# Kernel optimization log

Measured on AMD Instinct MI355X. Metric: run time of the kernel, lower is better.

## Reference

```python
import jax, jax.numpy as jnp
import numpy as np
from jax import lax

STRIDE = (1, 1)
PADDING = ((1, 1), (1, 1))


@jax.custom_vjp
def ternary_quantize(w):
    """Quantize OIHW weights to {-1,0,+1} with per-output-channel scale alpha."""
    abs_w = jnp.abs(w)
    delta = 0.7 * abs_w.mean(axis=(1, 2, 3), keepdims=True)          # [O,1,1,1]
    ternary = jnp.where(w > delta, 1.0, jnp.where(w < -delta, -1.0, 0.0)).astype(w.dtype)
    mask = ternary != 0
    count = jnp.maximum(mask.sum(axis=(1, 2, 3), keepdims=True), 1).astype(w.dtype)
    alpha = (abs_w * mask.astype(w.dtype)).sum(axis=(1, 2, 3), keepdims=True) / count
    return ternary, alpha


def _tq_fwd(w):
    return ternary_quantize(w), w


def _tq_bwd(w, grads):
    g_ternary, _g_alpha = grads  # STE: grad_alpha is discarded
    g = jnp.where(jnp.abs(w) > 1.0, 0.0, g_ternary)
    return (g,)


ternary_quantize.defvjp(_tq_fwd, _tq_bwd)


def setup_inputs() -> dict:
    key = jax.random.key(0)
    kx, kw = jax.random.split(key)
    x = jax.random.normal(kx, (32, 256, 56, 56), dtype=jnp.float32)
    # kaiming_normal fan_out: std = sqrt(2 / (out_ch * kH * kW))
    std = np.sqrt(2.0 / (256 * 3 * 3)).astype(np.float32)
    weight = jax.random.normal(kw, (256, 256, 3, 3), dtype=jnp.float32) * std
    return {"x": x, "weight": weight}


def reference(x, weight):
    ternary, alpha = ternary_quantize(weight)
    scaled_w = alpha * ternary  # values in {-alpha_o, 0, +alpha_o}
    return lax.conv_general_dilated(
        x, scaled_w,
        window_strides=STRIDE,
        padding=PADDING,
        dimension_numbers=("NCHW", "OIHW", "NCHW"),
    )
```

## Files before the change

### kernel.cpp

```cpp
#include <hip/hip_runtime.h>
#include <hip/hip_bf16.h>

typedef unsigned short u16;
typedef __bf16 bf16x8 __attribute__((ext_vector_type(8)));
typedef float f32x4 __attribute__((ext_vector_type(4)));
typedef u16 u16x8 __attribute__((ext_vector_type(8)));

__device__ __forceinline__ u16 f2bf(float f) {
    __bf16 h = (__bf16)f;
    return __builtin_bit_cast(unsigned short, h);
}

__device__ __forceinline__ void gl_lds16(const u16* g, u16* l) {
    __builtin_amdgcn_global_load_lds(
        (const __attribute__((address_space(1))) void*)g,
        (__attribute__((address_space(3))) void*)l, 16, 0, 0);
}

__device__ __forceinline__ void hard_barrier() {
    asm volatile("s_waitcnt vmcnt(0) lgkmcnt(0)" ::: "memory");
    __builtin_amdgcn_sched_barrier(0);
    __syncthreads();
}

__global__ __launch_bounds__(256) void prep_kernel(
        const float* __restrict__ x, const float* __restrict__ w,
        u16* __restrict__ xp, u16* __restrict__ wp,
        float* __restrict__ alpha) {
    __shared__ double red[4];
    __shared__ double red2[4];
    __shared__ int    redc[4];

    int bid = blockIdx.x;
    int t = threadIdx.x;

    if (bid < 256) {
        int o = bid;
        const float* wo = w + (size_t)o * 2304;
        float v[9];
        double asum = 0.0;
        #pragma unroll
        for (int i = 0; i < 9; ++i) { v[i] = wo[t * 9 + i]; asum += fabs((double)v[i]); }
        #pragma unroll
        for (int off = 32; off > 0; off >>= 1) asum += __shfl_down(asum, off, 64);
        int wv = t >> 6, lane = t & 63;
        if (lane == 0) red[wv] = asum;
        __syncthreads();
        double delta = 0.7 * ((red[0] + red[1] + red[2] + red[3]) / 2304.0);

        int mt = o >> 7, ol = o & 127;
        int ks = (t >> 3) & 7, c = t & 7;
        double msum = 0.0; int cnt = 0;
        #pragma unroll
        for (int i = 0; i < 9; ++i) {
            double f = (double)v[i];
            float tv = 0.f;
            if (f > delta) tv = 1.f;
            else if (f < -delta) tv = -1.f;
            if (tv != 0.f) { msum += fabs(f); cnt++; }
            int kc = i * 4 + (t >> 6);
            wp[((((size_t)mt * 36 + kc) * 8 + ks) * 128 + ol) * 8 + c] = f2bf(tv);
        }
        #pragma unroll
        for (int off = 32; off > 0; off >>= 1) {
            msum += __shfl_down(msum, off, 64);
            cnt  += __shfl_down(cnt,  off, 64);
        }
        if (lane == 0) { red2[wv] = msum; redc[wv] = cnt; }
        __syncthreads();
        if (t == 0) {
            double ms = red2[0] + red2[1] + red2[2] + red2[3];
            int cn = redc[0] + redc[1] + redc[2] + redc[3];
            alpha[o] = (float)(ms / (double)(cn > 0 ? cn : 1));
        }
        return;
    }

    int pbid = bid - 256;
    int img  = pbid & 31;
    int cihi = (pbid >> 5) & 31;
    int z    = pbid >> 10;

    if (z == 3 && t >= 16) {
        int bt = t - 16;
        if (bt < 228) {
            int hp, wl;
            if (bt < 58)       { hp = 0;            wl = bt; }
            else if (bt < 116) { hp = 57;           wl = bt - 58; }
            else if (bt < 172) { hp = bt - 116 + 1; wl = 0; }
            else               { hp = bt - 172 + 1; wl = 57; }
            u16x8 zv = {};
            *(u16x8*)(xp + (((size_t)(img * 32 + cihi) * 58 + hp) * 58 + wl) * 8) = zv;
        }
        return;
    }

    int slot = z * 256 + t;
    if (slot >= 784) return;
    int p = slot * 4;
    int h = p / 56, wq = p - h * 56;
    const float* xb = x + ((size_t)(img * 256 + cihi * 8)) * 3136 + p;
    f32x4 v[8];
    #pragma unroll
    for (int j = 0; j < 8; ++j) v[j] = *(const f32x4*)(xb + (size_t)j * 3136);
    u16* ob = xp + (((size_t)(img * 32 + cihi) * 58 + (h + 1)) * 58 + (wq + 1)) * 8;
    #pragma unroll
    for (int k = 0; k < 4; ++k) {
        u16x8 ov;
        #pragma unroll
        for (int j = 0; j < 8; ++j) ov[j] = f2bf(v[j][k]);
        *(u16x8*)(ob + k * 8) = ov;
    }
}

__global__ __launch_bounds__(256) void conv_gemm(
        const u16* __restrict__ Wp, const u16* __restrict__ Xp,
        const float* __restrict__ alpha, float* __restrict__ out) {
    __shared__ u16 lsA[8 * 128 * 8];
    __shared__ u16 lsB[8 * 128 * 8];

    int bid = blockIdx.x;
    int xcd = bid & 7, idx = bid >> 3;
    int mt = idx & 1;
    unsigned nt = (unsigned)(xcd * 98 + (idx >> 1));
    int o_base = mt * 128;
    unsigned sp_base = nt * 128u;

    int t = threadIdx.x;
    int lane = t & 63, wave = t >> 6;
    int wm = (wave >> 1) * 64, wn = (wave & 1) * 64;

    const u16* aTile = Wp + (size_t)mt * 294912;

    unsigned sp0 = sp_base + (unsigned)lane;
    unsigned sp1 = sp0 + 64u;
    unsigned img0 = sp0 / 3136u, rem0 = sp0 - img0 * 3136u;
    unsigned oh0 = rem0 / 56u,   ow0 = rem0 - oh0 * 56u;
    unsigned img1 = sp1 / 3136u, rem1 = sp1 - img1 * 3136u;
    unsigned oh1 = rem1 / 56u,   ow1 = rem1 - oh1 * 56u;
    const u16* bB0 = Xp + ((size_t)(img0 * 32) * 58 + oh0) * 58 * 8 + ow0 * 8;
    const u16* bB1 = Xp + ((size_t)(img1 * 32) * 58 + oh1) * 58 * 8 + ow1 * 8;

    int s0 = wave * 2, s1 = s0 + 1;
    u16* dB00 = lsB + (s0 * 128) * 8;
    u16* dB01 = lsB + (s0 * 128 + 64) * 8;
    u16* dB10 = lsB + (s1 * 128) * 8;
    u16* dB11 = lsB + (s1 * 128 + 64) * 8;

    f32x4 acc[4][4] = {};
    int row16 = lane & 15, quad = lane >> 4;

    for (int kc = 0; kc < 36; ++kc) {
        int f  = kc >> 2;
        int kh = f / 3, kw = f - kh * 3;
        int ci8 = (kc & 3) * 8;
        unsigned bhw = (unsigned)kh * 464u + (unsigned)kw * 8u;
        unsigned bo0 = (unsigned)(ci8 + s0) * 26912u + bhw;
        unsigned bo1 = (unsigned)(ci8 + s1) * 26912u + bhw;
        const u16* aC = aTile + kc * 8192;

        #pragma unroll
        for (int q = 0; q < 4; ++q) {
            int seg = wave * 4 + q;
            gl_lds16(aC + seg * 512 + lane * 8, lsA + seg * 512);
        }
        gl_lds16(bB0 + bo0, dB00);
        gl_lds16(bB1 + bo0, dB01);
        gl_lds16(bB0 + bo1, dB10);
        gl_lds16(bB1 + bo1, dB11);

        hard_barrier();

        #pragma unroll
        for (int kk = 0; kk < 2; ++kk) {
            int ks = kk * 4 + quad;
            bf16x8 af[4], bfr[4];
            #pragma unroll
            for (int i = 0; i < 4; ++i)
                af[i] = *(const bf16x8*)&lsA[(ks * 128 + wm + i * 16 + row16) * 8];
            #pragma unroll
            for (int j = 0; j < 4; ++j)
                bfr[j] = *(const bf16x8*)&lsB[(ks * 128 + wn + j * 16 + row16) * 8];
            #pragma unroll
            for (int i = 0; i < 4; ++i)
                #pragma unroll
                for (int j = 0; j < 4; ++j)
                    acc[i][j] = __builtin_amdgcn_mfma_f32_16x16x32_bf16(
                                    af[i], bfr[j], acc[i][j], 0, 0, 0);
        }

        hard_barrier();
    }

    int col = lane & 15;
    float al[4][4];
    #pragma unroll
    for (int i = 0; i < 4; ++i)
        #pragma unroll
        for (int rg = 0; rg < 4; ++rg)
            al[i][rg] = alpha[o_base + wm + i * 16 + quad * 4 + rg];

    #pragma unroll
    for (int j = 0; j < 4; ++j) {
        unsigned sp = sp_base + (unsigned)(wn + j * 16 + col);
        unsigned img = sp / 3136u;
        unsigned spi = sp - img * 3136u;
        float* ob = out + (size_t)img * 256 * 3136 + spi;
        #pragma unroll
        for (int i = 0; i < 4; ++i) {
            int o = o_base + wm + i * 16 + quad * 4;
            #pragma unroll
            for (int rg = 0; rg < 4; ++rg)
                ob[(size_t)(o + rg) * 3136] = acc[i][j][rg] * al[i][rg];
        }
    }
}

extern "C" void kernel_launch(void* const* d_in, const int* in_sizes, int n_in,
                              void* d_out, int out_size, void* d_ws, size_t ws_size,
                              hipStream_t stream) {
    const float* x = (const float*)d_in[0];
    const float* w = (const float*)d_in[1];
    float* out = (float*)d_out;

    char* ws = (char*)d_ws;
    u16*   xp    = (u16*)ws;
    u16*   wp    = (u16*)(ws + 55115776);
    float* alpha = (float*)(ws + 55115776 + 1179648);

    prep_kernel<<<4352, 256, 0, stream>>>(x, w, xp, wp, alpha);
    conv_gemm<<<784 * 2, 256, 0, stream>>>(wp, xp, alpha, out);
}
```

Baseline: 348.3 us.

## Double-buffer LDS tiles to overlap global loads with MFMA compute

Splits the A and B shared-memory tiles into two buffers. The global-to-LDS loads for the next K chunk are issued before the MFMAs on the current chunk, and each iteration ends with one barrier instead of two. The goal is to hide global load latency behind compute. It doubles LDS use to 64KB per block, which may lower occupancy. The barrier still waits on vmcnt(0), so the overlap only lasts for the duration of the compute.

```diff
diff --git a/kernel.cpp b/kernel.cpp
--- a/kernel.cpp
+++ b/kernel.cpp
@@ -116,8 +116,8 @@
 __global__ __launch_bounds__(256) void conv_gemm(
         const u16* __restrict__ Wp, const u16* __restrict__ Xp,
         const float* __restrict__ alpha, float* __restrict__ out) {
-    __shared__ u16 lsA[8 * 128 * 8];
-    __shared__ u16 lsB[8 * 128 * 8];
+    __shared__ u16 lsA[2][8 * 128 * 8];
+    __shared__ u16 lsB[2][8 * 128 * 8];
 
     int bid = blockIdx.x;
     int xcd = bid & 7, idx = bid >> 3;
@@ -142,15 +142,11 @@
     const u16* bB1 = Xp + ((size_t)(img1 * 32) * 58 + oh1) * 58 * 8 + ow1 * 8;
 
     int s0 = wave * 2, s1 = s0 + 1;
-    u16* dB00 = lsB + (s0 * 128) * 8;
-    u16* dB01 = lsB + (s0 * 128 + 64) * 8;
-    u16* dB10 = lsB + (s1 * 128) * 8;
-    u16* dB11 = lsB + (s1 * 128 + 64) * 8;
 
     f32x4 acc[4][4] = {};
     int row16 = lane & 15, quad = lane >> 4;
 
-    for (int kc = 0; kc < 36; ++kc) {
+    auto stage = [&](int kc, int buf) {
         int f  = kc >> 2;
         int kh = f / 3, kw = f - kh * 3;
         int ci8 = (kc & 3) * 8;
@@ -158,29 +154,36 @@
         unsigned bo0 = (unsigned)(ci8 + s0) * 26912u + bhw;
         unsigned bo1 = (unsigned)(ci8 + s1) * 26912u + bhw;
         const u16* aC = aTile + kc * 8192;
-
         #pragma unroll
         for (int q = 0; q < 4; ++q) {
             int seg = wave * 4 + q;
-            gl_lds16(aC + seg * 512 + lane * 8, lsA + seg * 512);
-        }
-        gl_lds16(bB0 + bo0, dB00);
-        gl_lds16(bB1 + bo0, dB01);
-        gl_lds16(bB0 + bo1, dB10);
-        gl_lds16(bB1 + bo1, dB11);
-
-        hard_barrier();
-
+            gl_lds16(aC + seg * 512 + lane * 8, &lsA[buf][seg * 512]);
+        }
+        gl_lds16(bB0 + bo0, &lsB[buf][s0 * 1024]);
+        gl_lds16(bB1 + bo0, &lsB[buf][s0 * 1024 + 512]);
+        gl_lds16(bB0 + bo1, &lsB[buf][s1 * 1024]);
+        gl_lds16(bB1 + bo1, &lsB[buf][s1 * 1024 + 512]);
+    };
+
+    stage(0, 0);
+    hard_barrier();
+
+    int cur = 0;
+    for (int kc = 0; kc < 36; ++kc) {
+        if (kc + 1 < 36) stage(kc + 1, cur ^ 1);
+
+        const u16* cA = lsA[cur];
+        const u16* cB = lsB[cur];
         #pragma unroll
         for (int kk = 0; kk < 2; ++kk) {
             int ks = kk * 4 + quad;
             bf16x8 af[4], bfr[4];
             #pragma unroll
             for (int i = 0; i < 4; ++i)
-                af[i] = *(const bf16x8*)&lsA[(ks * 128 + wm + i * 16 + row16) * 8];
+                af[i] = *(const bf16x8*)&cA[(ks * 128 + wm + i * 16 + row16) * 8];
             #pragma unroll
             for (int j = 0; j < 4; ++j)
-                bfr[j] = *(const bf16x8*)&lsB[(ks * 128 + wn + j * 16 + row16) * 8];
+                bfr[j] = *(const bf16x8*)&cB[(ks * 128 + wn + j * 16 + row16) * 8];
             #pragma unroll
             for (int i = 0; i < 4; ++i)
                 #pragma unroll
@@ -189,7 +192,10 @@
                                     af[i], bfr[j], acc[i][j], 0, 0, 0);
         }
 
-        hard_barrier();
+        if (kc + 1 < 36) {
+            hard_barrier();
+            cur ^= 1;
+        }
     }
 
     int col = lane & 15;
```

New measurement: 383.4 us. 1.1x slower.

## Double-buffer LDS tiles and overlap global loads with MFMA compute

Applied to the files above, without the earlier changes.

Replaces the single-buffer load/wait/compute loop with a two-stage ping-pong LDS pipeline. Each half-iteration reads fragments into registers, issues the async global-to-LDS loads for the chunk two steps ahead, then runs the MFMAs under raised wave priority. Partial vmcnt waits replace the full drains. This hides global load latency behind compute, at the cost of doubling LDS use and adding an occupancy hint of 2 blocks per CU via launch_bounds.

```diff
diff --git a/kernel.cpp b/kernel.cpp
--- a/kernel.cpp
+++ b/kernel.cpp
@@ -15,12 +15,6 @@
     __builtin_amdgcn_global_load_lds(
         (const __attribute__((address_space(1))) void*)g,
         (__attribute__((address_space(3))) void*)l, 16, 0, 0);
-}
-
-__device__ __forceinline__ void hard_barrier() {
-    asm volatile("s_waitcnt vmcnt(0) lgkmcnt(0)" ::: "memory");
-    __builtin_amdgcn_sched_barrier(0);
-    __syncthreads();
 }
 
 __global__ __launch_bounds__(256) void prep_kernel(
@@ -113,11 +107,66 @@
     }
 }
 
-__global__ __launch_bounds__(256) void conv_gemm(
+#define STAGE_CHUNK(KC, LA, LB) do {                                        \
+    int f_ = (KC) >> 2;                                                      \
+    int kh_ = f_ / 3, kw_ = f_ - kh_ * 3;                                    \
+    int ci8_ = ((KC) & 3) * 8;                                               \
+    unsigned bhw_ = (unsigned)kh_ * 464u + (unsigned)kw_ * 8u;               \
+    unsigned bo0_ = (unsigned)(ci8_ + s0) * 26912u + bhw_;                   \
+    unsigned bo1_ = (unsigned)(ci8_ + s1) * 26912u + bhw_;                   \
+    const u16* aC_ = aTile + (size_t)(KC) * 8192;                            \
+    _Pragma("unroll")                                                        \
+    for (int q_ = 0; q_ < 4; ++q_) {                                         \
+        int seg_ = wave * 4 + q_;                                            \
+        gl_lds16(aC_ + seg_ * 512 + lane * 8, (LA) + seg_ * 512);            \
+    }                                                                        \
+    gl_lds16(bB0 + bo0_, (LB) + s0 * 1024);                                  \
+    gl_lds16(bB1 + bo0_, (LB) + s0 * 1024 + 512);                            \
+    gl_lds16(bB0 + bo1_, (LB) + s1 * 1024);                                  \
+    gl_lds16(bB1 + bo1_, (LB) + s1 * 1024 + 512);                            \
+} while (0)
+
+#define HALF_ITER(LA, LB, VMSTR, STAGE_KC, DO_STAGE) do {                    \
+    asm volatile("s_waitcnt " VMSTR ::: "memory");                           \
+    __builtin_amdgcn_sched_barrier(0);                                       \
+    __builtin_amdgcn_s_barrier();                                            \
+    __builtin_amdgcn_sched_barrier(0);                                       \
+    bf16x8 af_[2][4], bf_[2][4];                                             \
+    _Pragma("unroll")                                                        \
+    for (int kk_ = 0; kk_ < 2; ++kk_) {                                      \
+        int ks_ = kk_ * 4 + quad;                                            \
+        _Pragma("unroll")                                                    \
+        for (int i_ = 0; i_ < 4; ++i_)                                       \
+            af_[kk_][i_] = *(const bf16x8*)&(LA)[(ks_ * 128 + wm + i_ * 16 + row16) * 8]; \
+        _Pragma("unroll")                                                    \
+        for (int j_ = 0; j_ < 4; ++j_)                                       \
+            bf_[kk_][j_] = *(const bf16x8*)&(LB)[(ks_ * 128 + wn + j_ * 16 + row16) * 8]; \
+    }                                                                        \
+    __builtin_amdgcn_sched_barrier(0);                                       \
+    asm volatile("s_waitcnt lgkmcnt(0)" ::: "memory");                       \
+    __builtin_amdgcn_sched_barrier(0);                                       \
+    __builtin_amdgcn_s_barrier();                                            \
+    __builtin_amdgcn_sched_barrier(0);                                       \
+    if (DO_STAGE) STAGE_CHUNK(STAGE_KC, LA, LB);                             \
+    __builtin_amdgcn_s_setprio(1);                                           \
+    _Pragma("unroll")                                                        \
+    for (int kk_ = 0; kk_ < 2; ++kk_)                                        \
+        _Pragma("unroll")                                                    \
+        for (int i_ = 0; i_ < 4; ++i_)                                       \
+            _Pragma("unroll")                                                \
+            for (int j_ = 0; j_ < 4; ++j_)                                   \
+                acc[i_][j_] = __builtin_amdgcn_mfma_f32_16x16x32_bf16(       \
+                                af_[kk_][i_], bf_[kk_][j_], acc[i_][j_], 0, 0, 0); \
+    __builtin_amdgcn_s_setprio(0);                                           \
+} while (0)
+
+__global__ __launch_bounds__(256, 2) void conv_gemm(
         const u16* __restrict__ Wp, const u16* __restrict__ Xp,
         const float* __restrict__ alpha, float* __restrict__ out) {
-    __shared__ u16 lsA[8 * 128 * 8];
-    __shared__ u16 lsB[8 * 128 * 8];
+    __shared__ u16 lsA0[8 * 128 * 8];
+    __shared__ u16 lsA1[8 * 128 * 8];
+    __shared__ u16 lsB0[8 * 128 * 8];
+    __shared__ u16 lsB1[8 * 128 * 8];
 
     int bid = blockIdx.x;
     int xcd = bid & 7, idx = bid >> 3;
@@ -142,55 +191,20 @@
     const u16* bB1 = Xp + ((size_t)(img1 * 32) * 58 + oh1) * 58 * 8 + ow1 * 8;
 
     int s0 = wave * 2, s1 = s0 + 1;
-    u16* dB00 = lsB + (s0 * 128) * 8;
-    u16* dB01 = lsB + (s0 * 128 + 64) * 8;
-    u16* dB10 = lsB + (s1 * 128) * 8;
-    u16* dB11 = lsB + (s1 * 128 + 64) * 8;
 
     f32x4 acc[4][4] = {};
     int row16 = lane & 15, quad = lane >> 4;
 
-    for (int kc = 0; kc < 36; ++kc) {
-        int f  = kc >> 2;
-        int kh = f / 3, kw = f - kh * 3;
-        int ci8 = (kc & 3) * 8;
-        unsigned bhw = (unsigned)kh * 464u + (unsigned)kw * 8u;
-        unsigned bo0 = (unsigned)(ci8 + s0) * 26912u + bhw;
-        unsigned bo1 = (unsigned)(ci8 + s1) * 26912u + bhw;
-        const u16* aC = aTile + kc * 8192;
-
-        #pragma unroll
-        for (int q = 0; q < 4; ++q) {
-            int seg = wave * 4 + q;
-            gl_lds16(aC + seg * 512 + lane * 8, lsA + seg * 512);
-        }
-        gl_lds16(bB0 + bo0, dB00);
-        gl_lds16(bB1 + bo0, dB01);
-        gl_lds16(bB0 + bo1, dB10);
-        gl_lds16(bB1 + bo1, dB11);
-
-        hard_barrier();
-
-        #pragma unroll
-        for (int kk = 0; kk < 2; ++kk) {
-            int ks = kk * 4 + quad;
-            bf16x8 af[4], bfr[4];
-            #pragma unroll
-            for (int i = 0; i < 4; ++i)
-                af[i] = *(const bf16x8*)&lsA[(ks * 128 + wm + i * 16 + row16) * 8];
-            #pragma unroll
-            for (int j = 0; j < 4; ++j)
-                bfr[j] = *(const bf16x8*)&lsB[(ks * 128 + wn + j * 16 + row16) * 8];
-            #pragma unroll
-            for (int i = 0; i < 4; ++i)
-                #pragma unroll
-                for (int j = 0; j < 4; ++j)
-                    acc[i][j] = __builtin_amdgcn_mfma_f32_16x16x32_bf16(
-                                    af[i], bfr[j], acc[i][j], 0, 0, 0);
-        }
-
-        hard_barrier();
-    }
+    STAGE_CHUNK(0, lsA0, lsB0);
+    STAGE_CHUNK(1, lsA1, lsB1);
+
+    #pragma unroll 1
+    for (int kc = 0; kc < 34; kc += 2) {
+        HALF_ITER(lsA0, lsB0, "vmcnt(8)", kc + 2, true);
+        HALF_ITER(lsA1, lsB1, "vmcnt(8)", kc + 3, true);
+    }
+    HALF_ITER(lsA0, lsB0, "vmcnt(8)", 0, false);
+    HALF_ITER(lsA1, lsB1, "vmcnt(0)", 0, false);
 
     int col = lane & 15;
     float al[4][4];
```

Result: faster. 307.6 us (-11.7%).
